# Kernel optimization log

Measured on AMD Instinct MI355X. Metric: run time of the kernel, lower is better.

Reference implementation:

```python
import jax, jax.numpy as jnp
import numpy as np

INPUT_SIZE = 512
HIDDEN = 1024
OUT_DIM = 256
N_SEQ = 64
SEQ_LEN = 512


def setup_inputs() -> dict:
    key = jax.random.key(0)
    ks = jax.random.split(key, 12)
    s_ih = 1.0 / np.sqrt(HIDDEN)
    inp = {
        "obs": jax.random.normal(ks[0], (N_SEQ * SEQ_LEN, INPUT_SIZE), jnp.float32),
        "h0": jax.random.normal(ks[1], (1, N_SEQ, HIDDEN), jnp.float32),
        "c0": jax.random.normal(ks[2], (1, N_SEQ, HIDDEN), jnp.float32),
        "episode_starts": (jax.random.uniform(ks[3], (N_SEQ * SEQ_LEN,)) < 0.05).astype(jnp.float32),
        # torch LSTM params, gate order i,f,g,o
        "W_ih": jax.random.uniform(ks[4], (4 * HIDDEN, INPUT_SIZE), jnp.float32, -s_ih, s_ih),
        "W_hh": jax.random.uniform(ks[5], (4 * HIDDEN, HIDDEN), jnp.float32, -s_ih, s_ih),
        "b_ih": jax.random.uniform(ks[6], (4 * HIDDEN,), jnp.float32, -s_ih, s_ih),
        "b_hh": jax.random.uniform(ks[7], (4 * HIDDEN,), jnp.float32, -s_ih, s_ih),
        "W_proj": jax.random.normal(ks[8], (HIDDEN, OUT_DIM), jnp.float32) * 0.02,
        "b_proj": jnp.zeros((OUT_DIM,), jnp.float32),
    }
    return inp


def _lstm_scan(x_tm, es_tm, h0, c0, W_ih, W_hh, b_ih, b_hh):
    """x_tm: [T, n_seq, in], es_tm: [T, n_seq]; per-step reset-masked LSTM."""
    Wi = W_ih.T  # [in, 4H]
    Wh = W_hh.T  # [H, 4H]
    b = b_ih + b_hh
    H = h0.shape[-1]

    def step(carry, inputs):
        h, c = carry  # [n_seq, H]
        x_t, es_t = inputs
        m = (1.0 - es_t)[:, None]
        h = h * m
        c = c * m
        gates = x_t @ Wi + h @ Wh + b  # [n_seq, 4H]
        i, f, g, o = jnp.split(gates, 4, axis=-1)
        i = jax.nn.sigmoid(i)
        f = jax.nn.sigmoid(f)
        g = jnp.tanh(g)
        o = jax.nn.sigmoid(o)
        c = f * c + i * g
        h = o * jnp.tanh(c)
        return (h, c), h

    (hT, cT), hs = jax.lax.scan(step, (h0, c0), (x_tm, es_tm))
    return hs, hT, cT  # hs: [T, n_seq, H]


def reference(obs, h0, c0, episode_starts, W_ih, W_hh, b_ih, b_hh, W_proj, b_proj):
    # FlattenExtractor: obs already flat [n_seq*T, input]
    feats = obs.reshape(N_SEQ, SEQ_LEN, INPUT_SIZE).swapaxes(0, 1)  # [T, n_seq, in]
    es = episode_starts.reshape(N_SEQ, SEQ_LEN).swapaxes(0, 1)      # [T, n_seq]
    hs, _, _ = _lstm_scan(feats, es, h0[0], c0[0], W_ih, W_hh, b_ih, b_hh)
    latent = hs.swapaxes(0, 1).reshape(N_SEQ * SEQ_LEN, HIDDEN)
    return latent @ W_proj + b_proj
```

## Files before the change

### kernel.cpp

```cpp
#include <hip/hip_runtime.h>

#define N_SEQ 64
#define T_LEN 512
#define IN_SZ 512
#define HID   1024
#define ODIM  256

#define REC_WGS  128
#define PROJ_WGS 16
#define TOT_WGS  (REC_WGS + PROJ_WGS)
#define BLK      256
#define RING_D   64
#define HSLOT    (N_SEQ * HID)

#define HBUF_OFF 4096

#define WF_OFF   0
#define CB_OFF   98304
#define GB_OFF   107008
#define BIAS_OFF 115456
#define LFLG_OFF 115584
#define GSTEP_OFF 115592
#define LDS_BYTES 115712
#define PWF_OFF 0
#define PB_OFF  32768
#define PGS_OFF 32832

typedef _Float16 half8  __attribute__((ext_vector_type(8)));
typedef float    f32x4  __attribute__((ext_vector_type(4)));
typedef float    f32x16 __attribute__((ext_vector_type(16)));

union U8B  { _Float16 h[4]; unsigned long long u; };

__device__ __forceinline__ float sigmf(float x) { return 1.f / (1.f + expf(-x)); }

__device__ __forceinline__ half8 cvt8(const float* p) {
  f32x4 v0 = *(const f32x4*)p;
  f32x4 v1 = *(const f32x4*)(p + 4);
  half8 h;
  h[0] = (_Float16)v0[0]; h[1] = (_Float16)v0[1];
  h[2] = (_Float16)v0[2]; h[3] = (_Float16)v0[3];
  h[4] = (_Float16)v1[0]; h[5] = (_Float16)v1[1];
  h[6] = (_Float16)v1[2]; h[7] = (_Float16)v1[3];
  return h;
}

#define ALOAD4(p) __hip_atomic_load((const int*)(p), __ATOMIC_RELAXED, __HIP_MEMORY_SCOPE_AGENT)

#define LEAD_POLL(tgt_) { for (;;) { \
    int m0_ = ALOAD4(arr + lane); \
    int m1_ = ALOAD4(arr + 64 + lane); \
    int m2_ = ALOAD4(arr + 128 + lane); \
    int m3_ = ALOAD4(arr + 192 + lane); \
    if (__all(min(min(m0_, m1_), min(m2_, m3_)) >= (tgt_))) break; \
    __builtin_amdgcn_s_sleep(1); } \
  asm volatile("" ::: "memory"); }

#define LDS_SPIN(ptr_, tgt_) { \
  while (__hip_atomic_load((ptr_), __ATOMIC_ACQUIRE, __HIP_MEMORY_SCOPE_WORKGROUP) < (tgt_)) {} \
  asm volatile("" ::: "memory"); }

__global__ void init_kernel(const float* __restrict__ h0, unsigned char* __restrict__ ws) {
  int gid = blockIdx.x * 256 + threadIdx.x;
  if (gid < 320) ((int*)ws)[gid] = -1;
  _Float16* hlast = (_Float16*)(ws + HBUF_OFF) + (size_t)(RING_D - 1) * HSLOT;
  if (gid < N_SEQ * HID) hlast[gid] = (_Float16)h0[gid];
}

__launch_bounds__(BLK, 1)
__global__ void lstm_coop(const float* __restrict__ obs,
                          const float* __restrict__ c0,
                          const float* __restrict__ es,
                          const float* __restrict__ W_ih,
                          const float* __restrict__ W_hh,
                          const float* __restrict__ b_ih,
                          const float* __restrict__ b_hh,
                          const float* __restrict__ W_proj,
                          const float* __restrict__ b_proj,
                          float* __restrict__ out,
                          unsigned char* __restrict__ ws) {
  extern __shared__ char smem[];
  const int tid = threadIdx.x, bid = blockIdx.x;
  const int w = tid >> 6, lane = tid & 63;
  int* arr  = (int*)ws;
  int* arrp = (int*)ws + 256;
  _Float16* hb = (_Float16*)(ws + HBUF_OFF);

  if (bid < REC_WGS) {
    const int wg = bid;
    _Float16* wf = (_Float16*)(smem + WF_OFF);
    float* cbuf  = (float*)(smem + CB_OFF);
    float* gbuf  = (float*)(smem + GB_OFF);
    float* bias  = (float*)(smem + BIAS_OFF);
    int*   lflg  = (int*)(smem + LFLG_OFF);
    int*   gstep = (int*)(smem + GSTEP_OFF);

    for (int idx = tid; idx < 96 * 64; idx += BLK) {
      int f = idx >> 6, l = idx & 63;
      int c = l & 31, kg = (l >> 5) * 8;
      int vk = f * 16 + kg;
      int grow = (c >> 3) * HID + wg * 8 + (c & 7);
      const float* src = (vk < IN_SZ)
          ? (W_ih + (size_t)grow * IN_SZ + vk)
          : (W_hh + (size_t)grow * HID + (vk - IN_SZ));
      _Float16* dst = wf + (size_t)idx * 8;
      #pragma unroll
      for (int j = 0; j < 8; ++j) dst[j] = (_Float16)src[j];
    }
    if (tid < 32) {
      int grow = (tid >> 3) * HID + wg * 8 + (tid & 7);
      bias[tid] = b_ih[grow] + b_hh[grow];
    }
    if (tid < 2) lflg[tid] = -1;
    if (tid == 0) *gstep = -1;
    __syncthreads();

    const int ch = w & 1;
    const int ks = w >> 1;
    const int col = lane & 31, kg = (lane >> 5) * 8;
    const int n_a = ch * 32 + col;

    if (ks == 0) {
      const int erow = lane >> 1, eq = lane & 1;
      const int n_e = ch * 32 + erow;
      const int hcb = wg * 8 + eq * 4;
      float cs[4];
      {
        f32x4 c4 = *(const f32x4*)(c0 + (size_t)n_e * HID + hcb);
        cs[0] = c4[0]; cs[1] = c4[1]; cs[2] = c4[2]; cs[3] = c4[3];
      }
      float* gb = gbuf + ch * 1056;

      for (int t = 0; t < T_LEN; ++t) {
        int ap = (t >= RING_D) ? ALOAD4(arrp + lane) : 0x7fffffff;
        float esv = es[(size_t)n_a * T_LEN + t];
        bool kill = (esv != 0.f);

        f32x16 acc = {};
        const float* xr = obs + ((size_t)n_a * T_LEN + t) * IN_SZ + kg;
        #pragma unroll
        for (int f = 0; f < 32; ++f) {
          half8 a = cvt8(xr + f * 16);
          half8 bv = *(const half8*)(wf + ((size_t)f * 64 + lane) * 8);
          acc = __builtin_amdgcn_mfma_f32_32x32x16_f16(a, bv, acc, 0, 0, 0);
        }

        if (t > 0) LDS_SPIN(gstep, t - 1);

        const _Float16* hrr = hb + (size_t)((t + RING_D - 1) & (RING_D - 1)) * HSLOT +
                              (size_t)n_a * HID + kg;
        #pragma unroll
        for (int f = 0; f < 16; ++f) {
          half8 a = *(const half8*)(hrr + f * 16);
          if (kill) a = (half8){};
          half8 bv = *(const half8*)(wf + ((size_t)(32 + f) * 64 + lane) * 8);
          acc = __builtin_amdgcn_mfma_f32_32x32x16_f16(a, bv, acc, 0, 0, 0);
        }

        while (__hip_atomic_load(&lflg[ch], __ATOMIC_ACQUIRE, __HIP_MEMORY_SCOPE_WORKGROUP) < t)
          __builtin_amdgcn_s_sleep(0);
        const float* cbc = cbuf + ch * 1088 + lane * 17;
        float tot[16];
        #pragma unroll
        for (int r = 0; r < 16; ++r) tot[r] = acc[r] + cbc[r];

        #pragma unroll
        for (int reg = 0; reg < 16; ++reg) {
          int r = (reg & 3) + 8 * (reg >> 2) + 4 * (lane >> 5);
          gb[r * 33 + col] = tot[reg];
        }
        asm volatile("s_waitcnt lgkmcnt(0)" ::: "memory");

        float m = 1.f - es[(size_t)n_e * T_LEN + t];
        U8B pk;
        #pragma unroll
        for (int p = 0; p < 4; ++p) {
          int j = eq * 4 + p;
          float pi = gb[erow * 33 + j]      + bias[j];
          float pf = gb[erow * 33 + 8 + j]  + bias[8 + j];
          float pg = gb[erow * 33 + 16 + j] + bias[16 + j];
          float po = gb[erow * 33 + 24 + j] + bias[24 + j];
          float cv = sigmf(pf) * (cs[p] * m) + sigmf(pi) * tanhf(pg);
          cs[p] = cv;
          pk.h[p] = (_Float16)(sigmf(po) * tanhf(cv));
        }

        if (t >= RING_D) {
          while (!__all(ap >= t - RING_D)) {
            __builtin_amdgcn_s_sleep(2);
            ap = ALOAD4(arrp + lane);
          }
        }

        __hip_atomic_store(
            (unsigned long long*)(hb + (size_t)(t & (RING_D - 1)) * HSLOT +
                                  (size_t)n_e * HID + hcb),
            pk.u, __ATOMIC_RELAXED, __HIP_MEMORY_SCOPE_AGENT);
        asm volatile("s_waitcnt vmcnt(0)" ::: "memory");
        if (lane == 0)
          __hip_atomic_store(arr + ch * 128 + wg, t, __ATOMIC_RELAXED, __HIP_MEMORY_SCOPE_AGENT);
      }
    } else {
      for (int t = 0; t < T_LEN; ++t) {
        float esv = es[(size_t)n_a * T_LEN + t];
        bool kill = (esv != 0.f);
        if (t > 0) {
          if (w == 2) {
            LEAD_POLL(t - 1);
            if (lane == 0)
              __hip_atomic_store(gstep, t - 1, __ATOMIC_RELEASE, __HIP_MEMORY_SCOPE_WORKGROUP);
          } else {
            LDS_SPIN(gstep, t - 1);
          }
        }

        const _Float16* hrr = hb + (size_t)((t + RING_D - 1) & (RING_D - 1)) * HSLOT +
                              (size_t)n_a * HID + 256 + kg;
        f32x16 acc = {};
        #pragma unroll
        for (int f = 0; f < 48; ++f) {
          half8 a = *(const half8*)(hrr + f * 16);
          if (kill) a = (half8){};
          half8 bv = *(const half8*)(wf + ((size_t)(48 + f) * 64 + lane) * 8);
          acc = __builtin_amdgcn_mfma_f32_32x32x16_f16(a, bv, acc, 0, 0, 0);
        }

        float* cbw = cbuf + ch * 1088 + lane * 17;
        *(f32x4*)(cbw + 0)  = (f32x4){acc[0],  acc[1],  acc[2],  acc[3]};
        *(f32x4*)(cbw + 4)  = (f32x4){acc[4],  acc[5],  acc[6],  acc[7]};
        *(f32x4*)(cbw + 8)  = (f32x4){acc[8],  acc[9],  acc[10], acc[11]};
        *(f32x4*)(cbw + 12) = (f32x4){acc[12], acc[13], acc[14], acc[15]};
        asm volatile("s_waitcnt lgkmcnt(0)" ::: "memory");
        if (lane == 0)
          __hip_atomic_store(&lflg[ch], t, __ATOMIC_RELEASE, __HIP_MEMORY_SCOPE_WORKGROUP);
      }
    }
  } else {
    const int p = bid - REC_WGS;
    const int pbase = p * 16;
    _Float16* pwf = (_Float16*)(smem + PWF_OFF);
    float* pb = (float*)(smem + PB_OFF);
    int* pgstep = (int*)(smem + PGS_OFF);
    for (int idx = tid; idx < 2048; idx += BLK) {
      int f = idx >> 6, l = idx & 63;
      int colp = pbase + (l & 15);
      int k0 = f * 32 + (l >> 4) * 8;
      _Float16* dst = pwf + (size_t)idx * 8;
      #pragma unroll
      for (int j = 0; j < 8; ++j)
        dst[j] = (_Float16)W_proj[(size_t)(k0 + j) * ODIM + colp];
    }
    if (tid < 16) pb[tid] = b_proj[pbase + tid];
    if (tid == 0) *pgstep = -1;
    __syncthreads();

    const int rq = w;
    const int n0 = rq * 16;
    const int arow = n0 + (lane & 15);
    const int kg8p = (lane >> 4) * 8;
    const float bz = pb[lane & 15];

    for (int t = 0; t < T_LEN; ++t) {
      if (w == 0) {
        LEAD_POLL(t);
        if (lane == 0)
          __hip_atomic_store(pgstep, t, __ATOMIC_RELEASE, __HIP_MEMORY_SCOPE_WORKGROUP);
      } else {
        LDS_SPIN(pgstep, t);
      }

      const _Float16* hr = hb + (size_t)(t & (RING_D - 1)) * HSLOT +
                           (size_t)arow * HID + kg8p;
      f32x4 acc = {};
      #pragma unroll
      for (int i = 0; i < 32; ++i) {
        half8 a = *(const half8*)(hr + i * 32);
        half8 bv = *(const half8*)(pwf + ((size_t)i * 64 + lane) * 8);
        acc = __builtin_amdgcn_mfma_f32_16x16x32_f16(a, bv, acc, 0, 0, 0);
      }
      #pragma unroll
      for (int r = 0; r < 4; ++r) {
        int nn = n0 + (lane >> 4) * 4 + r;
        out[((size_t)nn * T_LEN + t) * ODIM + pbase + (lane & 15)] = acc[r] + bz;
      }
      if (lane == 0)
        __hip_atomic_store(&arrp[p * 4 + w], t, __ATOMIC_RELAXED, __HIP_MEMORY_SCOPE_AGENT);
    }
  }
}

extern "C" void kernel_launch(void* const* d_in, const int* in_sizes, int n_in,
                              void* d_out, int out_size, void* d_ws, size_t ws_size,
                              hipStream_t stream) {
  const float* obs    = (const float*)d_in[0];
  const float* h0     = (const float*)d_in[1];
  const float* c0     = (const float*)d_in[2];
  const float* es     = (const float*)d_in[3];
  const float* W_ih   = (const float*)d_in[4];
  const float* W_hh   = (const float*)d_in[5];
  const float* b_ih   = (const float*)d_in[6];
  const float* b_hh   = (const float*)d_in[7];
  const float* W_proj = (const float*)d_in[8];
  const float* b_proj = (const float*)d_in[9];
  float* out = (float*)d_out;
  unsigned char* ws = (unsigned char*)d_ws;

  hipLaunchKernelGGL(init_kernel, dim3(256), dim3(256), 0, stream, h0, ws);

  hipFuncSetAttribute((const void*)lstm_coop,
                      hipFuncAttributeMaxDynamicSharedMemorySize, LDS_BYTES);

  void* args[] = { (void*)&obs, (void*)&c0, (void*)&es, (void*)&W_ih, (void*)&W_hh,
                   (void*)&b_ih, (void*)&b_hh, (void*)&W_proj, (void*)&b_proj,
                   (void*)&out, (void*)&ws };
  hipLaunchCooperativeKernel((const void*)lstm_coop, dim3(TOT_WGS), dim3(BLK),
                             args, LDS_BYTES, stream);
}
```

Measured before the change: 6.411 ms.

## Offload input projection to dedicated producer workgroups via global ring buffer

Adds 64 producer workgroups that compute the x·W_ih gate contributions ahead of time into a 16-deep global ring, with per-slot flags. The recurrent workgroups now hold only W_hh in LDS and split the hidden-state matmul evenly, 32 MFMAs per wave pair, instead of also doing the input GEMM on the critical path. Per-workgroup LDS leader polling is replaced by each wave polling only its own half's global flags. This takes the input projection off the serial recurrence, at the cost of extra global traffic, more co-resident workgroups, and more global polling.

Measured after the change: 8.244 ms. +28.6%, slower.

```diff
diff --git a/kernel.cpp b/kernel.cpp
--- a/kernel.cpp
+++ b/kernel.cpp
@@ -7,30 +7,32 @@
 #define ODIM  256
 
 #define REC_WGS  128
+#define GX_WGS   64
 #define PROJ_WGS 16
-#define TOT_WGS  (REC_WGS + PROJ_WGS)
+#define TOT_WGS  (REC_WGS + GX_WGS + PROJ_WGS)
 #define BLK      256
 #define RING_D   64
+#define GXD      16
 #define HSLOT    (N_SEQ * HID)
 
 #define HBUF_OFF 4096
+#define GX_OFF   8392704
 
 #define WF_OFF   0
-#define CB_OFF   98304
-#define GB_OFF   107008
-#define BIAS_OFF 115456
-#define LFLG_OFF 115584
-#define GSTEP_OFF 115592
-#define LDS_BYTES 115712
+#define CB_OFF   65536
+#define GB_OFF   74240
+#define BIAS_OFF 82688
+#define LFLG_OFF 82816
+#define LDS_BYTES 82944
 #define PWF_OFF 0
 #define PB_OFF  32768
-#define PGS_OFF 32832
 
 typedef _Float16 half8  __attribute__((ext_vector_type(8)));
 typedef float    f32x4  __attribute__((ext_vector_type(4)));
 typedef float    f32x16 __attribute__((ext_vector_type(16)));
 
 union U8B  { _Float16 h[4]; unsigned long long u; };
+union P2F  { float f[2]; unsigned long long u; };
 
 __device__ __forceinline__ float sigmf(float x) { return 1.f / (1.f + expf(-x)); }
 
@@ -46,23 +48,18 @@
 }
 
 #define ALOAD4(p) __hip_atomic_load((const int*)(p), __ATOMIC_RELAXED, __HIP_MEMORY_SCOPE_AGENT)
-
-#define LEAD_POLL(tgt_) { for (;;) { \
-    int m0_ = ALOAD4(arr + lane); \
-    int m1_ = ALOAD4(arr + 64 + lane); \
-    int m2_ = ALOAD4(arr + 128 + lane); \
-    int m3_ = ALOAD4(arr + 192 + lane); \
-    if (__all(min(min(m0_, m1_), min(m2_, m3_)) >= (tgt_))) break; \
+#define ASTORE8(p, v) __hip_atomic_store((unsigned long long*)(p), (v), __ATOMIC_RELAXED, __HIP_MEMORY_SCOPE_AGENT)
+
+#define POLL128(base_, tgt_) { for (;;) { \
+    int m0_ = ALOAD4((base_) + lane); \
+    int m1_ = ALOAD4((base_) + 64 + lane); \
+    if (__all(min(m0_, m1_) >= (tgt_))) break; \
     __builtin_amdgcn_s_sleep(1); } \
   asm volatile("" ::: "memory"); }
 
-#define LDS_SPIN(ptr_, tgt_) { \
-  while (__hip_atomic_load((ptr_), __ATOMIC_ACQUIRE, __HIP_MEMORY_SCOPE_WORKGROUP) < (tgt_)) {} \
-  asm volatile("" ::: "memory"); }
-
 __global__ void init_kernel(const float* __restrict__ h0, unsigned char* __restrict__ ws) {
   int gid = blockIdx.x * 256 + threadIdx.x;
-  if (gid < 320) ((int*)ws)[gid] = -1;
+  if (gid < 576) ((int*)ws)[gid] = -1;
   _Float16* hlast = (_Float16*)(ws + HBUF_OFF) + (size_t)(RING_D - 1) * HSLOT;
   if (gid < N_SEQ * HID) hlast[gid] = (_Float16)h0[gid];
 }
@@ -82,9 +79,11 @@
   extern __shared__ char smem[];
   const int tid = threadIdx.x, bid = blockIdx.x;
   const int w = tid >> 6, lane = tid & 63;
-  int* arr  = (int*)ws;
-  int* arrp = (int*)ws + 256;
+  int* arr   = (int*)ws;
+  int* arrp  = (int*)ws + 256;
+  int* gxarr = (int*)ws + 320;
   _Float16* hb = (_Float16*)(ws + HBUF_OFF);
+  float* gxb = (float*)(ws + GX_OFF);
 
   if (bid < REC_WGS) {
     const int wg = bid;
@@ -93,16 +92,12 @@
     float* gbuf  = (float*)(smem + GB_OFF);
     float* bias  = (float*)(smem + BIAS_OFF);
     int*   lflg  = (int*)(smem + LFLG_OFF);
-    int*   gstep = (int*)(smem + GSTEP_OFF);
-
-    for (int idx = tid; idx < 96 * 64; idx += BLK) {
+
+    for (int idx = tid; idx < 64 * 64; idx += BLK) {
       int f = idx >> 6, l = idx & 63;
-      int c = l & 31, kg = (l >> 5) * 8;
-      int vk = f * 16 + kg;
+      int c = l & 31, kk = f * 16 + ((l >> 5) * 8);
       int grow = (c >> 3) * HID + wg * 8 + (c & 7);
-      const float* src = (vk < IN_SZ)
-          ? (W_ih + (size_t)grow * IN_SZ + vk)
-          : (W_hh + (size_t)grow * HID + (vk - IN_SZ));
+      const float* src = W_hh + (size_t)grow * HID + kk;
       _Float16* dst = wf + (size_t)idx * 8;
       #pragma unroll
       for (int j = 0; j < 8; ++j) dst[j] = (_Float16)src[j];
@@ -112,18 +107,19 @@
       bias[tid] = b_ih[grow] + b_hh[grow];
     }
     if (tid < 2) lflg[tid] = -1;
-    if (tid == 0) *gstep = -1;
     __syncthreads();
 
     const int ch = w & 1;
     const int ks = w >> 1;
     const int col = lane & 31, kg = (lane >> 5) * 8;
     const int n_a = ch * 32 + col;
+    int* fl = arr + ch * 128;
 
     if (ks == 0) {
       const int erow = lane >> 1, eq = lane & 1;
       const int n_e = ch * 32 + erow;
       const int hcb = wg * 8 + eq * 4;
+      const int gxi = wg * 2 + ch;
       float cs[4];
       {
         f32x4 c4 = *(const f32x4*)(c0 + (size_t)n_e * HID + hcb);
@@ -136,33 +132,39 @@
         float esv = es[(size_t)n_a * T_LEN + t];
         bool kill = (esv != 0.f);
 
+        if (t > 0) POLL128(fl, t - 1);
+
+        const _Float16* hrr = hb + (size_t)((t + RING_D - 1) & (RING_D - 1)) * HSLOT +
+                              (size_t)n_a * HID + kg;
         f32x16 acc = {};
-        const float* xr = obs + ((size_t)n_a * T_LEN + t) * IN_SZ + kg;
         #pragma unroll
         for (int f = 0; f < 32; ++f) {
-          half8 a = cvt8(xr + f * 16);
+          half8 a = *(const half8*)(hrr + f * 16);
+          if (kill) a = (half8){};
           half8 bv = *(const half8*)(wf + ((size_t)f * 64 + lane) * 8);
           acc = __builtin_amdgcn_mfma_f32_32x32x16_f16(a, bv, acc, 0, 0, 0);
         }
 
-        if (t > 0) LDS_SPIN(gstep, t - 1);
-
-        const _Float16* hrr = hb + (size_t)((t + RING_D - 1) & (RING_D - 1)) * HSLOT +
-                              (size_t)n_a * HID + kg;
-        #pragma unroll
-        for (int f = 0; f < 16; ++f) {
-          half8 a = *(const half8*)(hrr + f * 16);
-          if (kill) a = (half8){};
-          half8 bv = *(const half8*)(wf + ((size_t)(32 + f) * 64 + lane) * 8);
-          acc = __builtin_amdgcn_mfma_f32_32x32x16_f16(a, bv, acc, 0, 0, 0);
-        }
+        while (ALOAD4(gxarr + gxi) < t) __builtin_amdgcn_s_sleep(1);
+        asm volatile("" ::: "memory");
+        const float* gxp = gxb + (((size_t)(t & (GXD - 1)) * 128 + wg) * 2 + ch) * 1024 +
+                           lane * 16;
+        f32x4 g0 = *(const f32x4*)(gxp + 0);
+        f32x4 g1 = *(const f32x4*)(gxp + 4);
+        f32x4 g2 = *(const f32x4*)(gxp + 8);
+        f32x4 g3 = *(const f32x4*)(gxp + 12);
 
         while (__hip_atomic_load(&lflg[ch], __ATOMIC_ACQUIRE, __HIP_MEMORY_SCOPE_WORKGROUP) < t)
           __builtin_amdgcn_s_sleep(0);
         const float* cbc = cbuf + ch * 1088 + lane * 17;
         float tot[16];
         #pragma unroll
-        for (int r = 0; r < 16; ++r) tot[r] = acc[r] + cbc[r];
+        for (int r = 0; r < 4; ++r) {
+          tot[r]      = acc[r]      + cbc[r]      + g0[r];
+          tot[4 + r]  = acc[4 + r]  + cbc[4 + r]  + g1[r];
+          tot[8 + r]  = acc[8 + r]  + cbc[8 + r]  + g2[r];
+          tot[12 + r] = acc[12 + r] + cbc[12 + r] + g3[r];
+        }
 
         #pragma unroll
         for (int reg = 0; reg < 16; ++reg) {
@@ -192,36 +194,25 @@
           }
         }
 
-        __hip_atomic_store(
-            (unsigned long long*)(hb + (size_t)(t & (RING_D - 1)) * HSLOT +
-                                  (size_t)n_e * HID + hcb),
-            pk.u, __ATOMIC_RELAXED, __HIP_MEMORY_SCOPE_AGENT);
+        ASTORE8(hb + (size_t)(t & (RING_D - 1)) * HSLOT + (size_t)n_e * HID + hcb, pk.u);
         asm volatile("s_waitcnt vmcnt(0)" ::: "memory");
         if (lane == 0)
-          __hip_atomic_store(arr + ch * 128 + wg, t, __ATOMIC_RELAXED, __HIP_MEMORY_SCOPE_AGENT);
+          __hip_atomic_store(fl + wg, t, __ATOMIC_RELAXED, __HIP_MEMORY_SCOPE_AGENT);
       }
     } else {
       for (int t = 0; t < T_LEN; ++t) {
         float esv = es[(size_t)n_a * T_LEN + t];
         bool kill = (esv != 0.f);
-        if (t > 0) {
-          if (w == 2) {
-            LEAD_POLL(t - 1);
-            if (lane == 0)
-              __hip_atomic_store(gstep, t - 1, __ATOMIC_RELEASE, __HIP_MEMORY_SCOPE_WORKGROUP);
-          } else {
-            LDS_SPIN(gstep, t - 1);
-          }
-        }
+        if (t > 0) POLL128(fl, t - 1);
 
         const _Float16* hrr = hb + (size_t)((t + RING_D - 1) & (RING_D - 1)) * HSLOT +
-                              (size_t)n_a * HID + 256 + kg;
+                              (size_t)n_a * HID + 512 + kg;
         f32x16 acc = {};
         #pragma unroll
-        for (int f = 0; f < 48; ++f) {
+        for (int f = 0; f < 32; ++f) {
           half8 a = *(const half8*)(hrr + f * 16);
           if (kill) a = (half8){};
-          half8 bv = *(const half8*)(wf + ((size_t)(48 + f) * 64 + lane) * 8);
+          half8 bv = *(const half8*)(wf + ((size_t)(32 + f) * 64 + lane) * 8);
           acc = __builtin_amdgcn_mfma_f32_32x32x16_f16(a, bv, acc, 0, 0, 0);
         }
 
@@ -235,12 +226,53 @@
           __hip_atomic_store(&lflg[ch], t, __ATOMIC_RELEASE, __HIP_MEMORY_SCOPE_WORKGROUP);
       }
     }
+  } else if (bid < REC_WGS + GX_WGS) {
+    const int g = bid - REC_WGS;
+    _Float16* wf = (_Float16*)(smem + WF_OFF);
+    for (int idx = tid; idx < 2 * 32 * 64; idx += BLK) {
+      int wgl = idx >> 11, f = (idx >> 6) & 31, l = idx & 63;
+      int c = l & 31, kk = f * 16 + ((l >> 5) * 8);
+      int grow = (c >> 3) * HID + (2 * g + wgl) * 8 + (c & 7);
+      const float* src = W_ih + (size_t)grow * IN_SZ + kk;
+      _Float16* dst = wf + (size_t)idx * 8;
+      #pragma unroll
+      for (int j = 0; j < 8; ++j) dst[j] = (_Float16)src[j];
+    }
+    __syncthreads();
+
+    const int wgl = w >> 1, ch = w & 1;
+    const int wg = 2 * g + wgl;
+    const int n_a = ch * 32 + (lane & 31);
+    const int kg = (lane >> 5) * 8;
+    const int gxi = wg * 2 + ch;
+
+    for (int t = 0; t < T_LEN; ++t) {
+      if (t >= GXD) {
+        while (ALOAD4(arr + ch * 128 + wg) < t - GXD) __builtin_amdgcn_s_sleep(2);
+      }
+      const float* xr = obs + ((size_t)n_a * T_LEN + t) * IN_SZ + kg;
+      f32x16 acc = {};
+      #pragma unroll
+      for (int f = 0; f < 32; ++f) {
+        half8 a = cvt8(xr + f * 16);
+        half8 bv = *(const half8*)(wf + ((size_t)(wgl * 32 + f) * 64 + lane) * 8);
+        acc = __builtin_amdgcn_mfma_f32_32x32x16_f16(a, bv, acc, 0, 0, 0);
+      }
+      float* gxp = gxb + (((size_t)(t & (GXD - 1)) * 128 + wg) * 2 + ch) * 1024 + lane * 16;
+      #pragma unroll
+      for (int i = 0; i < 8; ++i) {
+        P2F p; p.f[0] = acc[2 * i]; p.f[1] = acc[2 * i + 1];
+        ASTORE8((unsigned long long*)gxp + i, p.u);
+      }
+      asm volatile("s_waitcnt vmcnt(0)" ::: "memory");
+      if (lane == 0)
+        __hip_atomic_store(gxarr + gxi, t, __ATOMIC_RELAXED, __HIP_MEMORY_SCOPE_AGENT);
+    }
   } else {
-    const int p = bid - REC_WGS;
+    const int p = bid - REC_WGS - GX_WGS;
     const int pbase = p * 16;
     _Float16* pwf = (_Float16*)(smem + PWF_OFF);
     float* pb = (float*)(smem + PB_OFF);
-    int* pgstep = (int*)(smem + PGS_OFF);
     for (int idx = tid; idx < 2048; idx += BLK) {
       int f = idx >> 6, l = idx & 63;
       int colp = pbase + (l & 15);
@@ -251,23 +283,18 @@
         dst[j] = (_Float16)W_proj[(size_t)(k0 + j) * ODIM + colp];
     }
     if (tid < 16) pb[tid] = b_proj[pbase + tid];
-    if (tid == 0) *pgstep = -1;
     __syncthreads();
 
     const int rq = w;
+    const int ch = rq >> 1;
     const int n0 = rq * 16;
     const int arow = n0 + (lane & 15);
     const int kg8p = (lane >> 4) * 8;
     const float bz = pb[lane & 15];
+    int* fl = arr + ch * 128;
 
     for (int t = 0; t < T_LEN; ++t) {
-      if (w == 0) {
-        LEAD_POLL(t);
-        if (lane == 0)
-          __hip_atomic_store(pgstep, t, __ATOMIC_RELEASE, __HIP_MEMORY_SCOPE_WORKGROUP);
-      } else {
-        LDS_SPIN(pgstep, t);
-      }
+      POLL128(fl, t);
 
       const _Float16* hr = hb + (size_t)(t & (RING_D - 1)) * HSLOT +
                            (size_t)arow * HID + kg8p;
```

## Move input projection to producer waves with 4-deep LDS ring, split sync per batch half

Applied to the files above, without the earlier changes.

The recurrent waves now do the whole h@W_hh product themselves. The helper waves only compute the x@W_ih input contribution, running up to four timesteps ahead into a 4-slot LDS ring tracked by produce and consume flags. Each wave (and each projection wave) now polls only the 128 global flags of its own batch half instead of all 256 through one leader wave. The aim is to take the input GEMM off the serial critical path and to cut cross-workgroup synchronisation latency. The cost is that the critical-path wave now runs 64 MFMAs per step instead of 16 plus a split, and LDS use grows.

Measured after the change: 8.766 ms. +36.7%, slower.

```diff
diff --git a/kernel.cpp b/kernel.cpp
--- a/kernel.cpp
+++ b/kernel.cpp
@@ -11,20 +11,19 @@
 #define TOT_WGS  (REC_WGS + PROJ_WGS)
 #define BLK      256
 #define RING_D   64
+#define XD       4
 #define HSLOT    (N_SEQ * HID)
 
 #define HBUF_OFF 4096
 
 #define WF_OFF   0
-#define CB_OFF   98304
-#define GB_OFF   107008
-#define BIAS_OFF 115456
-#define LFLG_OFF 115584
-#define GSTEP_OFF 115592
-#define LDS_BYTES 115712
+#define CXR_OFF  98304
+#define GB_OFF   133120
+#define BIAS_OFF 141568
+#define XFLG_OFF 141696
+#define LDS_BYTES 141824
 #define PWF_OFF 0
 #define PB_OFF  32768
-#define PGS_OFF 32832
 
 typedef _Float16 half8  __attribute__((ext_vector_type(8)));
 typedef float    f32x4  __attribute__((ext_vector_type(4)));
@@ -46,18 +45,13 @@
 }
 
 #define ALOAD4(p) __hip_atomic_load((const int*)(p), __ATOMIC_RELAXED, __HIP_MEMORY_SCOPE_AGENT)
-
-#define LEAD_POLL(tgt_) { for (;;) { \
-    int m0_ = ALOAD4(arr + lane); \
-    int m1_ = ALOAD4(arr + 64 + lane); \
-    int m2_ = ALOAD4(arr + 128 + lane); \
-    int m3_ = ALOAD4(arr + 192 + lane); \
-    if (__all(min(min(m0_, m1_), min(m2_, m3_)) >= (tgt_))) break; \
+#define ASTORE8(p, v) __hip_atomic_store((unsigned long long*)(p), (v), __ATOMIC_RELAXED, __HIP_MEMORY_SCOPE_AGENT)
+
+#define POLL128(base_, tgt_) { for (;;) { \
+    int m0_ = ALOAD4((base_) + lane); \
+    int m1_ = ALOAD4((base_) + 64 + lane); \
+    if (__all(min(m0_, m1_) >= (tgt_))) break; \
     __builtin_amdgcn_s_sleep(1); } \
-  asm volatile("" ::: "memory"); }
-
-#define LDS_SPIN(ptr_, tgt_) { \
-  while (__hip_atomic_load((ptr_), __ATOMIC_ACQUIRE, __HIP_MEMORY_SCOPE_WORKGROUP) < (tgt_)) {} \
   asm volatile("" ::: "memory"); }
 
 __global__ void init_kernel(const float* __restrict__ h0, unsigned char* __restrict__ ws) {
@@ -89,20 +83,19 @@
   if (bid < REC_WGS) {
     const int wg = bid;
     _Float16* wf = (_Float16*)(smem + WF_OFF);
-    float* cbuf  = (float*)(smem + CB_OFF);
+    float* cxr   = (float*)(smem + CXR_OFF);
     float* gbuf  = (float*)(smem + GB_OFF);
     float* bias  = (float*)(smem + BIAS_OFF);
-    int*   lflg  = (int*)(smem + LFLG_OFF);
-    int*   gstep = (int*)(smem + GSTEP_OFF);
+    int*   xflg  = (int*)(smem + XFLG_OFF);
+    int*   xcons = (int*)(smem + XFLG_OFF) + 2;
 
     for (int idx = tid; idx < 96 * 64; idx += BLK) {
       int f = idx >> 6, l = idx & 63;
-      int c = l & 31, kg = (l >> 5) * 8;
-      int vk = f * 16 + kg;
+      int c = l & 31, kgl = (l >> 5) * 8;
       int grow = (c >> 3) * HID + wg * 8 + (c & 7);
-      const float* src = (vk < IN_SZ)
-          ? (W_ih + (size_t)grow * IN_SZ + vk)
-          : (W_hh + (size_t)grow * HID + (vk - IN_SZ));
+      const float* src = (f < 32)
+          ? (W_ih + (size_t)grow * IN_SZ + (f * 16 + kgl))
+          : (W_hh + (size_t)grow * HID + ((f - 32) * 16 + kgl));
       _Float16* dst = wf + (size_t)idx * 8;
       #pragma unroll
       for (int j = 0; j < 8; ++j) dst[j] = (_Float16)src[j];
@@ -111,16 +104,16 @@
       int grow = (tid >> 3) * HID + wg * 8 + (tid & 7);
       bias[tid] = b_ih[grow] + b_hh[grow];
     }
-    if (tid < 2) lflg[tid] = -1;
-    if (tid == 0) *gstep = -1;
+    if (tid < 4) ((int*)(smem + XFLG_OFF))[tid] = -1;
     __syncthreads();
 
     const int ch = w & 1;
-    const int ks = w >> 1;
+    const int role = w >> 1;
     const int col = lane & 31, kg = (lane >> 5) * 8;
     const int n_a = ch * 32 + col;
-
-    if (ks == 0) {
+    int* fl = arr + ch * 128;
+
+    if (role == 0) {
       const int erow = lane >> 1, eq = lane & 1;
       const int n_e = ch * 32 + erow;
       const int hcb = wg * 8 + eq * 4;
@@ -134,35 +127,30 @@
       for (int t = 0; t < T_LEN; ++t) {
         int ap = (t >= RING_D) ? ALOAD4(arrp + lane) : 0x7fffffff;
         float esv = es[(size_t)n_a * T_LEN + t];
+        float m = 1.f - es[(size_t)n_e * T_LEN + t];
         bool kill = (esv != 0.f);
 
-        f32x16 acc = {};
-        const float* xr = obs + ((size_t)n_a * T_LEN + t) * IN_SZ + kg;
-        #pragma unroll
-        for (int f = 0; f < 32; ++f) {
-          half8 a = cvt8(xr + f * 16);
-          half8 bv = *(const half8*)(wf + ((size_t)f * 64 + lane) * 8);
-          acc = __builtin_amdgcn_mfma_f32_32x32x16_f16(a, bv, acc, 0, 0, 0);
-        }
-
-        if (t > 0) LDS_SPIN(gstep, t - 1);
+        if (t > 0) POLL128(fl, t - 1);
 
         const _Float16* hrr = hb + (size_t)((t + RING_D - 1) & (RING_D - 1)) * HSLOT +
                               (size_t)n_a * HID + kg;
-        #pragma unroll
-        for (int f = 0; f < 16; ++f) {
+        f32x16 acc = {};
+        #pragma unroll
+        for (int f = 0; f < 64; ++f) {
           half8 a = *(const half8*)(hrr + f * 16);
           if (kill) a = (half8){};
           half8 bv = *(const half8*)(wf + ((size_t)(32 + f) * 64 + lane) * 8);
           acc = __builtin_amdgcn_mfma_f32_32x32x16_f16(a, bv, acc, 0, 0, 0);
         }
 
-        while (__hip_atomic_load(&lflg[ch], __ATOMIC_ACQUIRE, __HIP_MEMORY_SCOPE_WORKGROUP) < t)
+        while (__hip_atomic_load(&xflg[ch], __ATOMIC_ACQUIRE, __HIP_MEMORY_SCOPE_WORKGROUP) < t)
           __builtin_amdgcn_s_sleep(0);
-        const float* cbc = cbuf + ch * 1088 + lane * 17;
+        const float* cbc = cxr + ((ch * 4 + (t & 3)) * 1088) + lane * 17;
         float tot[16];
         #pragma unroll
         for (int r = 0; r < 16; ++r) tot[r] = acc[r] + cbc[r];
+        if (lane == 0)
+          __hip_atomic_store(&xcons[ch], t, __ATOMIC_RELEASE, __HIP_MEMORY_SCOPE_WORKGROUP);
 
         #pragma unroll
         for (int reg = 0; reg < 16; ++reg) {
@@ -171,7 +159,6 @@
         }
         asm volatile("s_waitcnt lgkmcnt(0)" ::: "memory");
 
-        float m = 1.f - es[(size_t)n_e * T_LEN + t];
         U8B pk;
         #pragma unroll
         for (int p = 0; p < 4; ++p) {
@@ -192,47 +179,34 @@
           }
         }
 
-        __hip_atomic_store(
-            (unsigned long long*)(hb + (size_t)(t & (RING_D - 1)) * HSLOT +
-                                  (size_t)n_e * HID + hcb),
-            pk.u, __ATOMIC_RELAXED, __HIP_MEMORY_SCOPE_AGENT);
+        ASTORE8(hb + (size_t)(t & (RING_D - 1)) * HSLOT + (size_t)n_e * HID + hcb, pk.u);
         asm volatile("s_waitcnt vmcnt(0)" ::: "memory");
         if (lane == 0)
-          __hip_atomic_store(arr + ch * 128 + wg, t, __ATOMIC_RELAXED, __HIP_MEMORY_SCOPE_AGENT);
+          __hip_atomic_store(fl + wg, t, __ATOMIC_RELAXED, __HIP_MEMORY_SCOPE_AGENT);
       }
     } else {
       for (int t = 0; t < T_LEN; ++t) {
-        float esv = es[(size_t)n_a * T_LEN + t];
-        bool kill = (esv != 0.f);
-        if (t > 0) {
-          if (w == 2) {
-            LEAD_POLL(t - 1);
-            if (lane == 0)
-              __hip_atomic_store(gstep, t - 1, __ATOMIC_RELEASE, __HIP_MEMORY_SCOPE_WORKGROUP);
-          } else {
-            LDS_SPIN(gstep, t - 1);
-          }
-        }
-
-        const _Float16* hrr = hb + (size_t)((t + RING_D - 1) & (RING_D - 1)) * HSLOT +
-                              (size_t)n_a * HID + 256 + kg;
+        if (t >= XD) {
+          while (__hip_atomic_load(&xcons[ch], __ATOMIC_ACQUIRE,
+                                   __HIP_MEMORY_SCOPE_WORKGROUP) < t - XD)
+            __builtin_amdgcn_s_sleep(1);
+        }
+        const float* xr = obs + ((size_t)n_a * T_LEN + t) * IN_SZ + kg;
         f32x16 acc = {};
         #pragma unroll
-        for (int f = 0; f < 48; ++f) {
-          half8 a = *(const half8*)(hrr + f * 16);
-          if (kill) a = (half8){};
-          half8 bv = *(const half8*)(wf + ((size_t)(48 + f) * 64 + lane) * 8);
+        for (int f = 0; f < 32; ++f) {
+          half8 a = cvt8(xr + f * 16);
+          half8 bv = *(const half8*)(wf + ((size_t)f * 64 + lane) * 8);
           acc = __builtin_amdgcn_mfma_f32_32x32x16_f16(a, bv, acc, 0, 0, 0);
         }
-
-        float* cbw = cbuf + ch * 1088 + lane * 17;
+        float* cbw = cxr + ((ch * 4 + (t & 3)) * 1088) + lane * 17;
         *(f32x4*)(cbw + 0)  = (f32x4){acc[0],  acc[1],  acc[2],  acc[3]};
         *(f32x4*)(cbw + 4)  = (f32x4){acc[4],  acc[5],  acc[6],  acc[7]};
         *(f32x4*)(cbw + 8)  = (f32x4){acc[8],  acc[9],  acc[10], acc[11]};
         *(f32x4*)(cbw + 12) = (f32x4){acc[12], acc[13], acc[14], acc[15]};
         asm volatile("s_waitcnt lgkmcnt(0)" ::: "memory");
         if (lane == 0)
-          __hip_atomic_store(&lflg[ch], t, __ATOMIC_RELEASE, __HIP_MEMORY_SCOPE_WORKGROUP);
+          __hip_atomic_store(&xflg[ch], t, __ATOMIC_RELEASE, __HIP_MEMORY_SCOPE_WORKGROUP);
       }
     }
   } else {
@@ -240,7 +214,6 @@
     const int pbase = p * 16;
     _Float16* pwf = (_Float16*)(smem + PWF_OFF);
     float* pb = (float*)(smem + PB_OFF);
-    int* pgstep = (int*)(smem + PGS_OFF);
     for (int idx = tid; idx < 2048; idx += BLK) {
       int f = idx >> 6, l = idx & 63;
       int colp = pbase + (l & 15);
@@ -251,23 +224,18 @@
         dst[j] = (_Float16)W_proj[(size_t)(k0 + j) * ODIM + colp];
     }
     if (tid < 16) pb[tid] = b_proj[pbase + tid];
-    if (tid == 0) *pgstep = -1;
     __syncthreads();
 
     const int rq = w;
+    const int ch = rq >> 1;
     const int n0 = rq * 16;
     const int arow = n0 + (lane & 15);
     const int kg8p = (lane >> 4) * 8;
     const float bz = pb[lane & 15];
+    int* fl = arr + ch * 128;
 
     for (int t = 0; t < T_LEN; ++t) {
-      if (w == 0) {
-        LEAD_POLL(t);
-        if (lane == 0)
-          __hip_atomic_store(pgstep, t, __ATOMIC_RELEASE, __HIP_MEMORY_SCOPE_WORKGROUP);
-      } else {
-        LDS_SPIN(pgstep, t);
-      }
+      POLL128(fl, t);
 
       const _Float16* hr = hb + (size_t)(t & (RING_D - 1)) * HSLOT +
                            (size_t)arow * HID + kg8p;
```
